# Kernel optimization log

Hardware: AMD Instinct MI355X
Metric: run time of the kernel (lower is better)

Reference implementation:

```python
import jax, jax.numpy as jnp
import numpy as np

N_ATOMS = 10000
N_EDGES = 250000
F_DIM = 128
N_RBF = 20
CUTOFF = 5.0
N_INT = 3
EPS = 1e-8


def setup_inputs() -> dict:
    key = jax.random.key(0)
    ks = jax.random.split(key, 16)
    inp = {}
    inp["atomic_numbers"] = jax.random.randint(ks[0], (N_ATOMS,), 1, 101)
    # positions in a 5 Angstrom box so many pairs lie inside the cutoff
    inp["R"] = jax.random.uniform(ks[1], (N_ATOMS, 3), dtype=jnp.float32) * 5.0
    idx_i = jnp.sort(jax.random.randint(ks[2], (N_EDGES,), 0, N_ATOMS))
    # ensure idx_j != idx_i so d_ij > 0
    idx_j = (idx_i + 1 + jax.random.randint(ks[3], (N_EDGES,), 0, N_ATOMS - 1)) % N_ATOMS
    inp["idx_i"] = idx_i
    inp["idx_j"] = idx_j
    inp["offsets"] = jnp.zeros((N_EDGES, 3), dtype=jnp.float32)

    def w(k, shape):
        fan_in = shape[-2]
        return jax.random.normal(k, shape, dtype=jnp.float32) / np.sqrt(fan_in).astype(np.float32)

    inp["emb"] = jax.random.normal(ks[4], (101, F_DIM), dtype=jnp.float32)
    inp["filt_W"] = w(ks[5], (N_RBF, 3 * F_DIM))
    inp["filt_b"] = jax.random.normal(ks[6], (3 * F_DIM,), dtype=jnp.float32) * 0.01
    inp["int_W1"] = w(ks[7], (N_INT, F_DIM, F_DIM))
    inp["int_b1"] = jnp.zeros((N_INT, 1, F_DIM), dtype=jnp.float32)
    inp["int_W2"] = w(ks[8], (N_INT, F_DIM, 3 * F_DIM))
    inp["int_b2"] = jnp.zeros((N_INT, 1, 3 * F_DIM), dtype=jnp.float32)
    inp["mix_Wmu"] = w(ks[9], (N_INT, F_DIM, 2 * F_DIM))
    inp["mix_W1"] = w(ks[10], (N_INT, 2 * F_DIM, F_DIM))
    inp["mix_b1"] = jnp.zeros((N_INT, 1, F_DIM), dtype=jnp.float32)
    inp["mix_W2"] = w(ks[11], (N_INT, F_DIM, 3 * F_DIM))
    inp["mix_b2"] = jnp.zeros((N_INT, 1, 3 * F_DIM), dtype=jnp.float32)
    return inp


def painn_forward(atomic_numbers, idx_i, idx_j, R, offsets, emb, filt_W, filt_b,
                  int_W1, int_b1, int_W2, int_b2,
                  mix_Wmu, mix_W1, mix_b1, mix_W2, mix_b2):
    n_atoms = atomic_numbers.shape[0]
    # geometry
    r_ij = R[idx_j] - R[idx_i] + offsets                      # [E,3]
    d_ij = jnp.linalg.norm(r_ij, axis=1, keepdims=True)       # [E,1]
    dir_ij = r_ij / d_ij                                      # [E,3]
    # Gaussian radial basis + cosine cutoff (schnetpack defaults)
    centers = jnp.linspace(0.0, CUTOFF, N_RBF, dtype=jnp.float32)
    coeff = -0.5 / (centers[1] - centers[0]) ** 2
    phi = jnp.exp(coeff * (d_ij[..., None] - centers) ** 2)   # [E,1,N_RBF]
    fcut = 0.5 * (jnp.cos(d_ij * (jnp.pi / CUTOFF)) + 1.0) * (d_ij < CUTOFF)  # [E,1]
    Wij = (phi @ filt_W + filt_b) * fcut[..., None]           # [E,1,3F] (shared filters)

    q = emb[atomic_numbers][:, None, :]                       # [N,1,F]
    mu = jnp.zeros((n_atoms, 3, F_DIM), dtype=q.dtype)        # [N,3,F]

    for i in range(N_INT):
        # ---- interaction (equivariant message passing) ----
        x = jax.nn.silu(q @ int_W1[i] + int_b1[i]) @ int_W2[i] + int_b2[i]  # [N,1,3F]
        xj = x[idx_j]                                          # [E,1,3F]
        muj = mu[idx_j]                                        # [E,3,F]
        xw = Wij * xj                                          # [E,1,3F]
        dq, dmuR, dmumu = jnp.split(xw, 3, axis=-1)            # each [E,1,F]
        dq = jax.ops.segment_sum(dq, idx_i, num_segments=n_atoms)          # [N,1,F]
        dmu = dmuR * dir_ij[..., None] + dmumu * muj           # [E,3,F]
        dmu = jax.ops.segment_sum(dmu, idx_i, num_segments=n_atoms)        # [N,3,F]
        q = q + dq
        mu = mu + dmu
        # ---- mixing (intra-atomic) ----
        mu_mix = mu @ mix_Wmu[i]                               # [N,3,2F]
        mu_V, mu_W = jnp.split(mu_mix, 2, axis=-1)             # [N,3,F] each
        mu_Vn = jnp.sqrt(jnp.sum(mu_V ** 2, axis=-2, keepdims=True) + EPS)  # [N,1,F]
        ctx = jnp.concatenate([q, mu_Vn], axis=-1)             # [N,1,2F]
        xm = jax.nn.silu(ctx @ mix_W1[i] + mix_b1[i]) @ mix_W2[i] + mix_b2[i]  # [N,1,3F]
        dq_intra, dmu_intra, dqmu_intra = jnp.split(xm, 3, axis=-1)
        dmu_intra = dmu_intra * mu_W                           # [N,3,F]
        dqmu_intra = dqmu_intra * jnp.sum(mu_V * mu_W, axis=1, keepdims=True)  # [N,1,F]
        q = q + dq_intra + dqmu_intra
        mu = mu + dmu_intra

    return q.squeeze(1), mu                                    # [N,F], [N,3,F]


def reference(atomic_numbers, R, idx_i, idx_j, offsets, emb, filt_W, filt_b,
              int_W1, int_b1, int_W2, int_b2,
              mix_Wmu, mix_W1, mix_b1, mix_W2, mix_b2):
    return painn_forward(atomic_numbers, idx_i, idx_j, R, offsets, emb, filt_W, filt_b,
                         int_W1, int_b1, int_W2, int_b2,
                         mix_Wmu, mix_W1, mix_b1, mix_W2, mix_b2)
```

## Files before the change

kernel.cpp:

```cpp
#include <hip/hip_runtime.h>
#include <math.h>

#define NA 10000
#define NE 250000
#define FD 128
#define NRBF 20
#define RCUT 5.0f

typedef _Float16 h16;
typedef __attribute__((ext_vector_type(8))) _Float16 half8;
typedef __attribute__((ext_vector_type(2))) _Float16 half2v;
typedef __attribute__((ext_vector_type(4))) float f32x4;

static __device__ __forceinline__ half8 f32x8_to_h8(const float* p) {
    float4 a = *(const float4*)p;
    float4 b = *(const float4*)(p + 4);
    half8 r;
    r[0] = (h16)a.x; r[1] = (h16)a.y; r[2] = (h16)a.z; r[3] = (h16)a.w;
    r[4] = (h16)b.x; r[5] = (h16)b.y; r[6] = (h16)b.z; r[7] = (h16)b.w;
    return r;
}
static __device__ __forceinline__ float silu(float v) {
    return v / (1.f + expf(-v));
}

__global__ __launch_bounds__(256) void setup_kernel(
    const float* __restrict__ R, const int* __restrict__ idx_i,
    const int* __restrict__ idx_j, const float* __restrict__ offsets,
    h16* __restrict__ ed, int* __restrict__ row_start,
    const float* __restrict__ int_W1, const float* __restrict__ int_W2,
    const float* __restrict__ mix_Wmu, const float* __restrict__ mix_W1,
    const float* __restrict__ mix_W2,
    h16* __restrict__ W1t, h16* __restrict__ W2t, h16* __restrict__ WmuT,
    h16* __restrict__ mW1t, h16* __restrict__ mW2t,
    const float* __restrict__ filt_W, const float* __restrict__ filt_b,
    h16* __restrict__ fwt)
{
    const int b = blockIdx.x;
    if (b < 977) {
        int e = b * 256 + threadIdx.x;
        if (e >= NE) return;
        int i = idx_i[e], j = idx_j[e];
        float rx = R[j * 3 + 0] - R[i * 3 + 0] + offsets[e * 3 + 0];
        float ry = R[j * 3 + 1] - R[i * 3 + 1] + offsets[e * 3 + 1];
        float rz = R[j * 3 + 2] - R[i * 3 + 2] + offsets[e * 3 + 2];
        float d = sqrtf(rx * rx + ry * ry + rz * rz);
        float inv = 1.f / d;
        float fcut = 0.f;
        if (d < RCUT) fcut = 0.5f * (cosf(d * (3.14159265358979323846f / RCUT)) + 1.f);
        h16* pp = ed + (size_t)e * 32;
        const float delta = RCUT / 19.f;
        const float coeff = -0.5f / (delta * delta);
#pragma unroll
        for (int r = 0; r < NRBF; ++r) {
            float dc = d - (float)r * delta;
            pp[r] = (h16)(expf(coeff * dc * dc) * fcut);
        }
        pp[20] = (h16)fcut;
        pp[21] = (h16)0.f; pp[22] = (h16)0.f; pp[23] = (h16)0.f;
        *(float4*)(pp + 24) = make_float4(rx * inv, ry * inv, rz * inv, 0.f);
    } else if (b < 1017) {
        int n = (b - 977) * 256 + threadIdx.x;
        if (n > NA) return;
        int lo = 0, hi = NE;
        while (lo < hi) {
            int mid = (lo + hi) >> 1;
            if (idx_i[mid] < n) lo = mid + 1; else hi = mid;
        }
        row_start[n] = lo;
    } else {
        int idx = (b - 1017) * 256 + threadIdx.x;
        if (idx < 49152) {
            int bt = idx >> 14, rem = idx & 16383;
            int nn = rem >> 7, kk = rem & 127;
            W1t[idx] = (h16)int_W1[(size_t)bt * 16384 + kk * 128 + nn];
        } else if ((idx -= 49152) < 147456) {
            int bt = idx / 49152, rem = idx - bt * 49152;
            int nn = rem >> 7, kk = rem & 127;
            W2t[idx] = (h16)int_W2[(size_t)bt * 49152 + kk * 384 + nn];
        } else if ((idx -= 147456) < 98304) {
            int bt = idx >> 15, rem = idx & 32767;
            int nn = rem >> 7, kk = rem & 127;
            WmuT[idx] = (h16)mix_Wmu[(size_t)bt * 32768 + kk * 256 + nn];
        } else if ((idx -= 98304) < 98304) {
            int bt = idx >> 15, rem = idx & 32767;
            int nn = rem >> 8, kk = rem & 255;
            mW1t[idx] = (h16)mix_W1[(size_t)bt * 32768 + kk * 128 + nn];
        } else if ((idx -= 98304) < 147456) {
            int bt = idx / 49152, rem = idx - bt * 49152;
            int nn = rem >> 7, kk = rem & 127;
            mW2t[idx] = (h16)mix_W2[(size_t)bt * 49152 + kk * 384 + nn];
        } else if ((idx -= 147456) < 12288) {
            int nn = idx >> 5, kk = idx & 31;
            float v = 0.f;
            if (kk < 20) v = filt_W[kk * 384 + nn];
            else if (kk == 20) v = filt_b[nn];
            fwt[idx] = (h16)v;
        }
    }
}

__global__ __launch_bounds__(256) void intmlp0_kernel(
    const int* __restrict__ Z, const float* __restrict__ emb, float* __restrict__ q,
    const h16* __restrict__ W1t, const float* __restrict__ b1,
    const h16* __restrict__ W2t, const float* __restrict__ b2, h16* __restrict__ x01c)
{
    __shared__ h16 Hs[16 * 136];
    const int tid = threadIdx.x;
    const int wave = tid >> 6, lane = tid & 63;
    const int ar = lane & 15, kg = lane >> 4;
    const size_t row0 = (size_t)blockIdx.x * 16;

    {
        int a = tid >> 4, f0 = (tid & 15) * 8;
        const float* src = emb + (size_t)Z[row0 + a] * 128 + f0;
        float4 v0 = *(const float4*)src;
        float4 v1 = *(const float4*)(src + 4);
        *(float4*)&q[(row0 + a) * 128 + f0] = v0;
        *(float4*)&q[(row0 + a) * 128 + f0 + 4] = v1;
    }
    const int zr = Z[row0 + ar];
    f32x4 a1[2] = {};
    for (int ks = 0; ks < 128; ks += 32) {
        int k = ks + kg * 8;
        half8 af = f32x8_to_h8(emb + (size_t)zr * 128 + k);
#pragma unroll
        for (int tt = 0; tt < 2; ++tt) {
            int t = wave * 2 + tt;
            half8 bf = *(const half8*)&W1t[(size_t)(t * 16 + ar) * 128 + k];
            a1[tt] = __builtin_amdgcn_mfma_f32_16x16x32_f16(af, bf, a1[tt], 0, 0, 0);
        }
    }
#pragma unroll
    for (int tt = 0; tt < 2; ++tt) {
        int col = (wave * 2 + tt) * 16 + ar;
        float bb = b1[col];
#pragma unroll
        for (int r = 0; r < 4; ++r)
            Hs[(kg * 4 + r) * 136 + col] = (h16)silu(a1[tt][r] + bb);
    }
    __syncthreads();
    f32x4 a2[6] = {};
    for (int ks = 0; ks < 128; ks += 32) {
        int k = ks + kg * 8;
        half8 af = *(const half8*)&Hs[ar * 136 + k];
#pragma unroll
        for (int tt = 0; tt < 6; ++tt) {
            int t = wave * 6 + tt;
            half8 bf = *(const half8*)&W2t[(size_t)(t * 16 + ar) * 128 + k];
            a2[tt] = __builtin_amdgcn_mfma_f32_16x16x32_f16(af, bf, a2[tt], 0, 0, 0);
        }
    }
#pragma unroll
    for (int tt = 0; tt < 6; ++tt) {
        int col = (wave * 6 + tt) * 16 + ar;
        if (col < 256) {
            float bb = b2[col];
            int slot = col >> 7, ff = col & 127;
#pragma unroll
            for (int r = 0; r < 4; ++r)
                x01c[((row0 + kg * 4 + r) * 128 + ff) * 2 + slot] = (h16)(a2[tt][r] + bb);
        }
    }
}

template<bool HAS_MU>
__global__ __launch_bounds__(128, 4) void edge_kernel(
    const h16* __restrict__ ed, const h16* __restrict__ fwt,
    const int* __restrict__ row_start, const int* __restrict__ idx_j,
    const h16* __restrict__ gat, const float* __restrict__ mup,
    float* __restrict__ mun, h16* __restrict__ mu16n, float* __restrict__ q)
{
    const int n = blockIdx.x, f = threadIdx.x;
    half8 FA[3], FB[3], FC[3];
    {
        const half8* pa = (const half8*)(fwt + (size_t)f * 32);
        const half8* pb = (const half8*)(fwt + (size_t)(128 + f) * 32);
#pragma unroll
        for (int r = 0; r < 3; ++r) { FA[r] = pa[r]; FB[r] = pb[r]; }
        if (HAS_MU) {
            const half8* pc = (const half8*)(fwt + (size_t)(256 + f) * 32);
#pragma unroll
            for (int r = 0; r < 3; ++r) FC[r] = pc[r];
        }
    }
    asm volatile("" : "+v"(FA[0]), "+v"(FA[1]), "+v"(FA[2]),
                      "+v"(FB[0]), "+v"(FB[1]), "+v"(FB[2]));
    if (HAS_MU)
        asm volatile("" : "+v"(FC[0]), "+v"(FC[1]), "+v"(FC[2]));

    half2v fa[12], fb[12], fc[12];
    *(half8*)&fa[0] = FA[0]; *(half8*)&fa[4] = FA[1]; *(half8*)&fa[8] = FA[2];
    *(half8*)&fb[0] = FB[0]; *(half8*)&fb[4] = FB[1]; *(half8*)&fb[8] = FB[2];
    if (HAS_MU) {
        *(half8*)&fc[0] = FC[0]; *(half8*)&fc[4] = FC[1]; *(half8*)&fc[8] = FC[2];
    }

    const size_t rstr = HAS_MU ? 768 : 256;
    const h16* xmf = gat + (HAS_MU ? (size_t)f * 6 : (size_t)f * 2);
    float accq = 0.f, am0 = 0.f, am1 = 0.f, am2 = 0.f;
    const int e0 = row_start[n], e1 = row_start[n + 1];
    if (e0 < e1) {
        int j = idx_j[e0];
        const unsigned* gp = (const unsigned*)(xmf + (size_t)j * rstr);
        unsigned g0n = gp[0], g1n = 0u, g2n = 0u;
        if (HAS_MU) { g1n = gp[1]; g2n = gp[2]; }
        const h16* pb8 = ed + (size_t)e0 * 32;
        half8 p0n = *(const half8*)pb8;
        half8 p1n = *(const half8*)(pb8 + 8);
        half8 p2n = *(const half8*)(pb8 + 16);
        float4 dn = *(const float4*)(pb8 + 24);
        for (int e = e0; e < e1; ++e) {
            unsigned g0 = g0n, g1 = g1n, g2 = g2n;
            half8 p0 = p0n, p1 = p1n, p2 = p2n;
            float4 g = dn;
            int ep = (e + 1 < e1) ? e + 1 : e;
            int j2 = idx_j[ep];
            const unsigned* gp2 = (const unsigned*)(xmf + (size_t)j2 * rstr);
            g0n = gp2[0];
            if (HAS_MU) { g1n = gp2[1]; g2n = gp2[2]; }
            const h16* pb2 = ed + (size_t)ep * 32;
            p0n = *(const half8*)pb2;
            p1n = *(const half8*)(pb2 + 8);
            p2n = *(const half8*)(pb2 + 16);
            dn = *(const float4*)(pb2 + 24);
            half2v pr[12];
            *(half8*)&pr[0] = p0; *(half8*)&pr[4] = p1; *(half8*)&pr[8] = p2;
            half2v A0 = {(h16)0.f, (h16)0.f}, A1 = A0, A2 = A0;
#pragma unroll
            for (int r = 0; r < 11; ++r) {
                A0 = pr[r] * fa[r] + A0;
                A1 = pr[r] * fb[r] + A1;
                if (HAS_MU) A2 = pr[r] * fc[r] + A2;
            }
            float w0 = (float)A0[0] + (float)A0[1];
            float w1 = (float)A1[0] + (float)A1[1];
            half2v h01 = __builtin_bit_cast(half2v, g0);
            half2v h23 = __builtin_bit_cast(half2v, g1);
            float x0 = (float)h01[0], x1 = (float)h01[1];
            accq = fmaf(w0, x0, accq);
            float xw1 = w1 * x1;
            if (HAS_MU) {
                float w2 = (float)A2[0] + (float)A2[1];
                half2v h45 = __builtin_bit_cast(half2v, g2);
                float x2 = (float)h23[0];
                float xw2 = w2 * x2;
                am0 += xw1 * g.x + xw2 * (float)h23[1];
                am1 += xw1 * g.y + xw2 * (float)h45[0];
                am2 += xw1 * g.z + xw2 * (float)h45[1];
            } else {
                am0 = fmaf(xw1, g.x, am0);
                am1 = fmaf(xw1, g.y, am1);
                am2 = fmaf(xw1, g.z, am2);
            }
        }
    }

    q[(size_t)n * FD + f] += accq;
    size_t b = (size_t)n * 384;
    float m0 = (HAS_MU ? mup[b + f] : 0.f) + am0;
    float m1 = (HAS_MU ? mup[b + 128 + f] : 0.f) + am1;
    float m2 = (HAS_MU ? mup[b + 256 + f] : 0.f) + am2;
    mun[b + f] = m0; mun[b + 128 + f] = m1; mun[b + 256 + f] = m2;
    mu16n[b + f] = (h16)m0; mu16n[b + 128 + f] = (h16)m1; mu16n[b + 256 + f] = (h16)m2;
}

__global__ __launch_bounds__(256) void mixint_kernel(
    const h16* __restrict__ mu16n, const h16* __restrict__ WmuT,
    const h16* __restrict__ W1t, const float* __restrict__ b1,
    const h16* __restrict__ W2t, const float* __restrict__ b2,
    float* __restrict__ q, float* __restrict__ mu, h16* __restrict__ xmw,
    const h16* __restrict__ nW1t, const float* __restrict__ nb1,
    const h16* __restrict__ nW2t, const float* __restrict__ nb2)
{
    __shared__ __align__(16) h16 MM[48 * 264];
    __shared__ h16 CT[16 * 264];
    __shared__ h16 Hs[16 * 136];
    __shared__ h16 XM[16 * 392];
    const int tid = threadIdx.x;
    const int wave = tid >> 6, lane = tid & 63;
    const int ar = lane & 15, kg = lane >> 4;
    const size_t row0 = (size_t)blockIdx.x * 16;

    {
        f32x4 acc[3][4] = {};
        int aloc[3], dloc[3];
#pragma unroll
        for (int rt = 0; rt < 3; ++rt) {
            int rr = rt * 16 + ar;
            aloc[rt] = rr / 3;
            dloc[rt] = rr - 3 * aloc[rt];
        }
        for (int ks = 0; ks < 128; ks += 32) {
            int k = ks + kg * 8;
            half8 afr[3];
#pragma unroll
            for (int rt = 0; rt < 3; ++rt)
                afr[rt] = *(const half8*)&mu16n[(row0 + aloc[rt]) * 384 + dloc[rt] * 128 + k];
#pragma unroll
            for (int ct = 0; ct < 4; ++ct) {
                int cc = wave * 4 + ct;
                half8 bf = *(const half8*)&WmuT[(size_t)(cc * 16 + ar) * 128 + k];
#pragma unroll
                for (int rt = 0; rt < 3; ++rt)
                    acc[rt][ct] = __builtin_amdgcn_mfma_f32_16x16x32_f16(afr[rt], bf, acc[rt][ct], 0, 0, 0);
            }
        }
#pragma unroll
        for (int rt = 0; rt < 3; ++rt)
#pragma unroll
            for (int ct = 0; ct < 4; ++ct) {
                int col = (wave * 4 + ct) * 16 + ar;
#pragma unroll
                for (int r = 0; r < 4; ++r)
                    MM[(rt * 16 + kg * 4 + r) * 264 + col] = (h16)acc[rt][ct][r];
            }
    }
    __syncthreads();

    {
        int a = tid >> 4, fi = (tid & 15) * 8;
        const float* qp = q + (row0 + a) * 128 + fi;
        float4 q0 = *(const float4*)qp;
        float4 q1 = *(const float4*)(qp + 4);
        float qv[8] = {q0.x, q0.y, q0.z, q0.w, q1.x, q1.y, q1.z, q1.w};
#pragma unroll
        for (int jj = 0; jj < 8; ++jj) {
            int ff = fi + jj;
            float v0 = (float)MM[(a * 3 + 0) * 264 + ff];
            float v1 = (float)MM[(a * 3 + 1) * 264 + ff];
            float v2 = (float)MM[(a * 3 + 2) * 264 + ff];
            CT[a * 264 + 128 + ff] = (h16)sqrtf(v0 * v0 + v1 * v1 + v2 * v2 + 1e-8f);
            CT[a * 264 + ff] = (h16)qv[jj];
        }
    }
    __syncthreads();

    {
        f32x4 a1[2] = {};
        for (int ks = 0; ks < 256; ks += 32) {
            int k = ks + kg * 8;
            half8 af = *(const half8*)&CT[ar * 264 + k];
#pragma unroll
            for (int tt = 0; tt < 2; ++tt) {
                int t = wave * 2 + tt;
                half8 bf = *(const half8*)&W1t[(size_t)(t * 16 + ar) * 256 + k];
                a1[tt] = __builtin_amdgcn_mfma_f32_16x16x32_f16(af, bf, a1[tt], 0, 0, 0);
            }
        }
#pragma unroll
        for (int tt = 0; tt < 2; ++tt) {
            int col = (wave * 2 + tt) * 16 + ar;
            float bb = b1[col];
#pragma unroll
            for (int r = 0; r < 4; ++r)
                Hs[(kg * 4 + r) * 136 + col] = (h16)silu(a1[tt][r] + bb);
        }
    }
    __syncthreads();

    {
        f32x4 a2[6] = {};
        for (int ks = 0; ks < 128; ks += 32) {
            int k = ks + kg * 8;
            half8 af = *(const half8*)&Hs[ar * 136 + k];
#pragma unroll
            for (int tt = 0; tt < 6; ++tt) {
                int t = wave * 6 + tt;
                half8 bf = *(const half8*)&W2t[(size_t)(t * 16 + ar) * 128 + k];
                a2[tt] = __builtin_amdgcn_mfma_f32_16x16x32_f16(af, bf, a2[tt], 0, 0, 0);
            }
        }
#pragma unroll
        for (int tt = 0; tt < 6; ++tt) {
            int col = (wave * 6 + tt) * 16 + ar;
            float bb = b2[col];
#pragma unroll
            for (int r = 0; r < 4; ++r)
                XM[(kg * 4 + r) * 392 + col] = (h16)(a2[tt][r] + bb);
        }
    }
    __syncthreads();

    h16 mh[24];
    {
        int a = tid >> 4, fi = (tid & 15) * 8;
        size_t n = row0 + a;
#pragma unroll
        for (int jj = 0; jj < 8; ++jj) {
            int ff = fi + jj;
            float dq  = (float)XM[a * 392 + ff];
            float dm  = (float)XM[a * 392 + 128 + ff];
            float dqm = (float)XM[a * 392 + 256 + ff];
            float v0 = (float)MM[(a * 3 + 0) * 264 + ff], w0 = (float)MM[(a * 3 + 0) * 264 + 128 + ff];
            float v1 = (float)MM[(a * 3 + 1) * 264 + ff], w1 = (float)MM[(a * 3 + 1) * 264 + 128 + ff];
            float v2 = (float)MM[(a * 3 + 2) * 264 + ff], w2 = (float)MM[(a * 3 + 2) * 264 + 128 + ff];
            float sv = v0 * w0 + v1 * w1 + v2 * w2;
            float qn = q[n * 128 + ff] + dq + dqm * sv;
            q[n * 128 + ff] = qn;
            CT[a * 264 + ff] = (h16)qn;
            size_t b = n * 384 + ff;
            float m0 = mu[b] + dm * w0;
            float m1 = mu[b + 128] + dm * w1;
            float m2 = mu[b + 256] + dm * w2;
            mu[b] = m0; mu[b + 128] = m1; mu[b + 256] = m2;
            mh[jj * 3 + 0] = (h16)m0; mh[jj * 3 + 1] = (h16)m1; mh[jj * 3 + 2] = (h16)m2;
        }
    }
    if (!nW1t) return;
    __syncthreads();

    {
        f32x4 a1[2] = {};
        for (int ks = 0; ks < 128; ks += 32) {
            int k = ks + kg * 8;
            half8 af = *(const half8*)&CT[ar * 264 + k];
#pragma unroll
            for (int tt = 0; tt < 2; ++tt) {
                int t = wave * 2 + tt;
                half8 bf = *(const half8*)&nW1t[(size_t)(t * 16 + ar) * 128 + k];
                a1[tt] = __builtin_amdgcn_mfma_f32_16x16x32_f16(af, bf, a1[tt], 0, 0, 0);
            }
        }
#pragma unroll
        for (int tt = 0; tt < 2; ++tt) {
            int col = (wave * 2 + tt) * 16 + ar;
            float bb = nb1[col];
#pragma unroll
            for (int r = 0; r < 4; ++r)
                Hs[(kg * 4 + r) * 136 + col] = (h16)silu(a1[tt][r] + bb);
        }
        __syncthreads();
        f32x4 a2[6] = {};
        for (int ks = 0; ks < 128; ks += 32) {
            int k = ks + kg * 8;
            half8 af = *(const half8*)&Hs[ar * 136 + k];
#pragma unroll
            for (int tt = 0; tt < 6; ++tt) {
                int t = wave * 6 + tt;
                half8 bf = *(const half8*)&nW2t[(size_t)(t * 16 + ar) * 128 + k];
                a2[tt] = __builtin_amdgcn_mfma_f32_16x16x32_f16(af, bf, a2[tt], 0, 0, 0);
            }
        }
        h16* XMP = MM;
#pragma unroll
        for (int tt = 0; tt < 6; ++tt) {
            int col = (wave * 6 + tt) * 16 + ar;
            float bb = nb2[col];
            int slot = col >> 7, ff = col & 127;
#pragma unroll
            for (int r = 0; r < 4; ++r)
                XMP[((kg * 4 + r) * 128 + ff) * 6 + slot] = (h16)(a2[tt][r] + bb);
        }
        {
            int a = tid >> 4, fi = (tid & 15) * 8;
#pragma unroll
            for (int jj = 0; jj < 8; ++jj)
#pragma unroll
                for (int s = 0; s < 3; ++s)
                    XMP[(a * 128 + fi + jj) * 6 + 3 + s] = mh[jj * 3 + s];
        }
        __syncthreads();
        {
            const uint4* src = (const uint4*)MM;
            uint4* dst = (uint4*)(xmw + row0 * 768);
#pragma unroll
            for (int i = 0; i < 6; ++i)
                dst[tid + i * 256] = src[tid + i * 256];
        }
    }
}

extern "C" void kernel_launch(void* const* d_in, const int* in_sizes, int n_in,
                              void* d_out, int out_size, void* d_ws, size_t ws_size,
                              hipStream_t stream)
{
    const int*   Z       = (const int*)d_in[0];
    const float* R       = (const float*)d_in[1];
    const int*   idx_i   = (const int*)d_in[2];
    const int*   idx_j   = (const int*)d_in[3];
    const float* offsets = (const float*)d_in[4];
    const float* emb     = (const float*)d_in[5];
    const float* filt_W  = (const float*)d_in[6];
    const float* filt_b  = (const float*)d_in[7];
    const float* int_W1  = (const float*)d_in[8];
    const float* int_b1  = (const float*)d_in[9];
    const float* int_W2  = (const float*)d_in[10];
    const float* int_b2  = (const float*)d_in[11];
    const float* mix_Wmu = (const float*)d_in[12];
    const float* mix_W1  = (const float*)d_in[13];
    const float* mix_b1  = (const float*)d_in[14];
    const float* mix_W2  = (const float*)d_in[15];
    const float* mix_b2  = (const float*)d_in[16];

    float* q_out  = (float*)d_out;
    float* mu_out = (float*)d_out + (size_t)NA * FD;

    char* base = (char*)d_ws;
    size_t o = 0;
    auto alloc = [&](size_t bytes) -> void* {
        void* p = base + o;
        o += (bytes + 255) & ~(size_t)255;
        return p;
    };
    h16*   ed     = (h16*)alloc((size_t)NE * 32 * 2);
    h16*   xm     = (h16*)alloc((size_t)NA * 128 * 6 * 2);
    h16*   x01c   = (h16*)alloc((size_t)NA * 128 * 2 * 2);
    h16*   mu16p  = (h16*)alloc((size_t)NA * 384 * 2);
    float* mu_ws  = (float*)alloc((size_t)NA * 384 * 4);
    h16*   W1t    = (h16*)alloc((size_t)3 * 128 * 128 * 2);
    h16*   W2t    = (h16*)alloc((size_t)3 * 384 * 128 * 2);
    h16*   WmuT   = (h16*)alloc((size_t)3 * 256 * 128 * 2);
    h16*   mW1t   = (h16*)alloc((size_t)3 * 128 * 256 * 2);
    h16*   mW2t   = (h16*)alloc((size_t)3 * 384 * 128 * 2);
    h16*   fwt    = (h16*)alloc((size_t)384 * 32 * 2);
    int*   row_st = (int*)alloc((size_t)(NA + 1) * 4);

    setup_kernel<<<3177, 256, 0, stream>>>(R, idx_i, idx_j, offsets, ed, row_st,
                                           int_W1, int_W2, mix_Wmu, mix_W1, mix_W2,
                                           W1t, W2t, WmuT, mW1t, mW2t,
                                           filt_W, filt_b, fwt);

    intmlp0_kernel<<<NA / 16, 256, 0, stream>>>(Z, emb, q_out,
                                                W1t, int_b1, W2t, int_b2, x01c);
    edge_kernel<false><<<NA, 128, 0, stream>>>(ed, fwt, row_st, idx_j,
                                               x01c, nullptr, mu_out, mu16p, q_out);
    mixint_kernel<<<NA / 16, 256, 0, stream>>>(
        mu16p, WmuT, mW1t, mix_b1, mW2t, mix_b2, q_out, mu_out, xm,
        W1t + 16384, int_b1 + 128, W2t + 49152, int_b2 + 384);

    edge_kernel<true><<<NA, 128, 0, stream>>>(ed, fwt, row_st, idx_j,
                                              xm, mu_out, mu_ws, mu16p, q_out);
    mixint_kernel<<<NA / 16, 256, 0, stream>>>(
        mu16p, WmuT + 32768, mW1t + 32768, mix_b1 + 128, mW2t + 49152, mix_b2 + 384,
        q_out, mu_ws, xm,
        W1t + 32768, int_b1 + 256, W2t + 98304, int_b2 + 768);

    edge_kernel<true><<<NA, 128, 0, stream>>>(ed, fwt, row_st, idx_j,
                                              xm, mu_ws, mu_out, mu16p, q_out);
    mixint_kernel<<<NA / 16, 256, 0, stream>>>(
        mu16p, WmuT + 65536, mW1t + 65536, mix_b1 + 256, mW2t + 98304, mix_b2 + 768,
        q_out, mu_out, xm,
        nullptr, nullptr, nullptr, nullptr);
}
```

Before: 424.8 us.

## Compute first interaction MLP per element type instead of per atom

In the first interaction block the features depend only on atomic number, so the MLP now runs over the 101 embedding rows rather than all 10000 atoms. The neighbour's atomic number is packed into a spare slot of the per-edge record, so the first edge pass indexes the small per-type table directly without reading idx_j. The q initialisation moves into the setup kernel, and the mixing kernel reuses q values already held in registers instead of reloading them. This removes most of the first MLP's work and cuts gather traffic, at the cost of a more tangled setup kernel and an fp16 bit-cast trick to store an integer.

```diff
diff --git a/kernel.cpp b/kernel.cpp
--- a/kernel.cpp
+++ b/kernel.cpp
@@ -27,6 +27,7 @@
 __global__ __launch_bounds__(256) void setup_kernel(
     const float* __restrict__ R, const int* __restrict__ idx_i,
     const int* __restrict__ idx_j, const float* __restrict__ offsets,
+    const int* __restrict__ Zt, const float* __restrict__ emb, float* __restrict__ q,
     h16* __restrict__ ed, int* __restrict__ row_start,
     const float* __restrict__ int_W1, const float* __restrict__ int_W2,
     const float* __restrict__ mix_Wmu, const float* __restrict__ mix_W1,
@@ -57,7 +58,9 @@
             pp[r] = (h16)(expf(coeff * dc * dc) * fcut);
         }
         pp[20] = (h16)fcut;
-        pp[21] = (h16)0.f; pp[22] = (h16)0.f; pp[23] = (h16)0.f;
+        pp[21] = (h16)0.f;
+        pp[22] = __builtin_bit_cast(h16, (unsigned short)Zt[j]);
+        pp[23] = (h16)0.f;
         *(float4*)(pp + 24) = make_float4(rx * inv, ry * inv, rz * inv, 0.f);
     } else if (b < 1017) {
         int n = (b - 977) * 256 + threadIdx.x;
@@ -68,7 +71,7 @@
             if (idx_i[mid] < n) lo = mid + 1; else hi = mid;
         }
         row_start[n] = lo;
-    } else {
+    } else if (b < 3177) {
         int idx = (b - 1017) * 256 + threadIdx.x;
         if (idx < 49152) {
             int bt = idx >> 14, rem = idx & 16383;
@@ -97,29 +100,31 @@
             else if (kk == 20) v = filt_b[nn];
             fwt[idx] = (h16)v;
         }
-    }
-}
-
-__global__ __launch_bounds__(256) void intmlp0_kernel(
-    const int* __restrict__ Z, const float* __restrict__ emb, float* __restrict__ q,
+    } else {
+        int a = (b - 3177) * 16 + (threadIdx.x >> 4);
+        int f0 = (threadIdx.x & 15) * 8;
+        if (a < NA) {
+            const float* src = emb + (size_t)Zt[a] * 128 + f0;
+            float4 v0 = *(const float4*)src;
+            float4 v1 = *(const float4*)(src + 4);
+            *(float4*)&q[(size_t)a * 128 + f0] = v0;
+            *(float4*)&q[(size_t)a * 128 + f0 + 4] = v1;
+        }
+    }
+}
+
+__global__ __launch_bounds__(256) void intmlp0z_kernel(
+    const float* __restrict__ emb,
     const h16* __restrict__ W1t, const float* __restrict__ b1,
-    const h16* __restrict__ W2t, const float* __restrict__ b2, h16* __restrict__ x01c)
+    const h16* __restrict__ W2t, const float* __restrict__ b2, h16* __restrict__ x01z)
 {
     __shared__ h16 Hs[16 * 136];
     const int tid = threadIdx.x;
     const int wave = tid >> 6, lane = tid & 63;
     const int ar = lane & 15, kg = lane >> 4;
-    const size_t row0 = (size_t)blockIdx.x * 16;
-
-    {
-        int a = tid >> 4, f0 = (tid & 15) * 8;
-        const float* src = emb + (size_t)Z[row0 + a] * 128 + f0;
-        float4 v0 = *(const float4*)src;
-        float4 v1 = *(const float4*)(src + 4);
-        *(float4*)&q[(row0 + a) * 128 + f0] = v0;
-        *(float4*)&q[(row0 + a) * 128 + f0 + 4] = v1;
-    }
-    const int zr = Z[row0 + ar];
+    const int row0 = blockIdx.x * 16;
+
+    const int zr = min(row0 + ar, 100);
     f32x4 a1[2] = {};
     for (int ks = 0; ks < 128; ks += 32) {
         int k = ks + kg * 8;
@@ -158,8 +163,11 @@
             float bb = b2[col];
             int slot = col >> 7, ff = col & 127;
 #pragma unroll
-            for (int r = 0; r < 4; ++r)
-                x01c[((row0 + kg * 4 + r) * 128 + ff) * 2 + slot] = (h16)(a2[tt][r] + bb);
+            for (int r = 0; r < 4; ++r) {
+                int z = row0 + kg * 4 + r;
+                if (z <= 100)
+                    x01z[((size_t)z * 128 + ff) * 2 + slot] = (h16)(a2[tt][r] + bb);
+            }
         }
     }
 }
@@ -196,59 +204,94 @@
         *(half8*)&fc[0] = FC[0]; *(half8*)&fc[4] = FC[1]; *(half8*)&fc[8] = FC[2];
     }
 
-    const size_t rstr = HAS_MU ? 768 : 256;
-    const h16* xmf = gat + (HAS_MU ? (size_t)f * 6 : (size_t)f * 2);
     float accq = 0.f, am0 = 0.f, am1 = 0.f, am2 = 0.f;
     const int e0 = row_start[n], e1 = row_start[n + 1];
-    if (e0 < e1) {
-        int j = idx_j[e0];
-        const unsigned* gp = (const unsigned*)(xmf + (size_t)j * rstr);
-        unsigned g0n = gp[0], g1n = 0u, g2n = 0u;
-        if (HAS_MU) { g1n = gp[1]; g2n = gp[2]; }
-        const h16* pb8 = ed + (size_t)e0 * 32;
-        half8 p0n = *(const half8*)pb8;
-        half8 p1n = *(const half8*)(pb8 + 8);
-        half8 p2n = *(const half8*)(pb8 + 16);
-        float4 dn = *(const float4*)(pb8 + 24);
-        for (int e = e0; e < e1; ++e) {
-            unsigned g0 = g0n, g1 = g1n, g2 = g2n;
-            half8 p0 = p0n, p1 = p1n, p2 = p2n;
-            float4 g = dn;
-            int ep = (e + 1 < e1) ? e + 1 : e;
-            int j2 = idx_j[ep];
-            const unsigned* gp2 = (const unsigned*)(xmf + (size_t)j2 * rstr);
-            g0n = gp2[0];
-            if (HAS_MU) { g1n = gp2[1]; g2n = gp2[2]; }
-            const h16* pb2 = ed + (size_t)ep * 32;
-            p0n = *(const half8*)pb2;
-            p1n = *(const half8*)(pb2 + 8);
-            p2n = *(const half8*)(pb2 + 16);
-            dn = *(const float4*)(pb2 + 24);
-            half2v pr[12];
-            *(half8*)&pr[0] = p0; *(half8*)&pr[4] = p1; *(half8*)&pr[8] = p2;
-            half2v A0 = {(h16)0.f, (h16)0.f}, A1 = A0, A2 = A0;
-#pragma unroll
-            for (int r = 0; r < 11; ++r) {
-                A0 = pr[r] * fa[r] + A0;
-                A1 = pr[r] * fb[r] + A1;
-                if (HAS_MU) A2 = pr[r] * fc[r] + A2;
-            }
-            float w0 = (float)A0[0] + (float)A0[1];
-            float w1 = (float)A1[0] + (float)A1[1];
-            half2v h01 = __builtin_bit_cast(half2v, g0);
-            half2v h23 = __builtin_bit_cast(half2v, g1);
-            float x0 = (float)h01[0], x1 = (float)h01[1];
-            accq = fmaf(w0, x0, accq);
-            float xw1 = w1 * x1;
-            if (HAS_MU) {
+
+    if (HAS_MU) {
+        const h16* xmf = gat + (size_t)f * 6;
+        if (e0 < e1) {
+            int j = idx_j[e0];
+            const unsigned* gp = (const unsigned*)(xmf + (size_t)j * 768);
+            unsigned g0n = gp[0], g1n = gp[1], g2n = gp[2];
+            const h16* pb8 = ed + (size_t)e0 * 32;
+            half8 p0n = *(const half8*)pb8;
+            half8 p1n = *(const half8*)(pb8 + 8);
+            half8 p2n = *(const half8*)(pb8 + 16);
+            float4 dn = *(const float4*)(pb8 + 24);
+            for (int e = e0; e < e1; ++e) {
+                unsigned g0 = g0n, g1 = g1n, g2 = g2n;
+                half8 p0 = p0n, p1 = p1n, p2 = p2n;
+                float4 g = dn;
+                int ep = (e + 1 < e1) ? e + 1 : e;
+                int j2 = idx_j[ep];
+                const unsigned* gp2 = (const unsigned*)(xmf + (size_t)j2 * 768);
+                g0n = gp2[0]; g1n = gp2[1]; g2n = gp2[2];
+                const h16* pb2 = ed + (size_t)ep * 32;
+                p0n = *(const half8*)pb2;
+                p1n = *(const half8*)(pb2 + 8);
+                p2n = *(const half8*)(pb2 + 16);
+                dn = *(const float4*)(pb2 + 24);
+                half2v pr[12];
+                *(half8*)&pr[0] = p0; *(half8*)&pr[4] = p1; *(half8*)&pr[8] = p2;
+                half2v A0 = {(h16)0.f, (h16)0.f}, A1 = A0, A2 = A0;
+#pragma unroll
+                for (int r = 0; r < 11; ++r) {
+                    A0 = pr[r] * fa[r] + A0;
+                    A1 = pr[r] * fb[r] + A1;
+                    A2 = pr[r] * fc[r] + A2;
+                }
+                float w0 = (float)A0[0] + (float)A0[1];
+                float w1 = (float)A1[0] + (float)A1[1];
                 float w2 = (float)A2[0] + (float)A2[1];
+                half2v h01 = __builtin_bit_cast(half2v, g0);
+                half2v h23 = __builtin_bit_cast(half2v, g1);
                 half2v h45 = __builtin_bit_cast(half2v, g2);
+                float x0 = (float)h01[0], x1 = (float)h01[1];
+                accq = fmaf(w0, x0, accq);
+                float xw1 = w1 * x1;
                 float x2 = (float)h23[0];
                 float xw2 = w2 * x2;
                 am0 += xw1 * g.x + xw2 * (float)h23[1];
                 am1 += xw1 * g.y + xw2 * (float)h45[0];
                 am2 += xw1 * g.z + xw2 * (float)h45[1];
-            } else {
+            }
+        }
+    } else {
+        const h16* xmf = gat + (size_t)f * 2;
+        if (e0 < e1) {
+            const h16* pb8 = ed + (size_t)e0 * 32;
+            half8 p0n = *(const half8*)pb8;
+            half8 p1n = *(const half8*)(pb8 + 8);
+            half8 p2n = *(const half8*)(pb8 + 16);
+            float4 dn = *(const float4*)(pb8 + 24);
+            unsigned short z0 = __builtin_bit_cast(unsigned short, (h16)p2n[6]);
+            unsigned g0n = *(const unsigned*)(xmf + (size_t)z0 * 256);
+            for (int e = e0; e < e1; ++e) {
+                unsigned g0 = g0n;
+                half8 p0 = p0n, p1 = p1n, p2 = p2n;
+                float4 g = dn;
+                int ep = (e + 1 < e1) ? e + 1 : e;
+                const h16* pb2 = ed + (size_t)ep * 32;
+                p0n = *(const half8*)pb2;
+                p1n = *(const half8*)(pb2 + 8);
+                p2n = *(const half8*)(pb2 + 16);
+                dn = *(const float4*)(pb2 + 24);
+                unsigned short z2 = __builtin_bit_cast(unsigned short, (h16)p2n[6]);
+                g0n = *(const unsigned*)(xmf + (size_t)z2 * 256);
+                half2v pr[12];
+                *(half8*)&pr[0] = p0; *(half8*)&pr[4] = p1; *(half8*)&pr[8] = p2;
+                half2v A0 = {(h16)0.f, (h16)0.f}, A1 = A0;
+#pragma unroll
+                for (int r = 0; r < 11; ++r) {
+                    A0 = pr[r] * fa[r] + A0;
+                    A1 = pr[r] * fb[r] + A1;
+                }
+                float w0 = (float)A0[0] + (float)A0[1];
+                float w1 = (float)A1[0] + (float)A1[1];
+                half2v h01 = __builtin_bit_cast(half2v, g0);
+                float x0 = (float)h01[0], x1 = (float)h01[1];
+                accq = fmaf(w0, x0, accq);
+                float xw1 = w1 * x1;
                 am0 = fmaf(xw1, g.x, am0);
                 am1 = fmaf(xw1, g.y, am1);
                 am2 = fmaf(xw1, g.z, am2);
@@ -318,12 +361,14 @@
     }
     __syncthreads();
 
+    float qv[8];
     {
         int a = tid >> 4, fi = (tid & 15) * 8;
         const float* qp = q + (row0 + a) * 128 + fi;
         float4 q0 = *(const float4*)qp;
         float4 q1 = *(const float4*)(qp + 4);
-        float qv[8] = {q0.x, q0.y, q0.z, q0.w, q1.x, q1.y, q1.z, q1.w};
+        qv[0] = q0.x; qv[1] = q0.y; qv[2] = q0.z; qv[3] = q0.w;
+        qv[4] = q1.x; qv[5] = q1.y; qv[6] = q1.z; qv[7] = q1.w;
 #pragma unroll
         for (int jj = 0; jj < 8; ++jj) {
             int ff = fi + jj;
@@ -396,7 +441,7 @@
             float v1 = (float)MM[(a * 3 + 1) * 264 + ff], w1 = (float)MM[(a * 3 + 1) * 264 + 128 + ff];
             float v2 = (float)MM[(a * 3 + 2) * 264 + ff], w2 = (float)MM[(a * 3 + 2) * 264 + 128 + ff];
             float sv = v0 * w0 + v1 * w1 + v2 * w2;
-            float qn = q[n * 128 + ff] + dq + dqm * sv;
+            float qn = qv[jj] + dq + dqm * sv;
             q[n * 128 + ff] = qn;
             CT[a * 264 + ff] = (h16)qn;
             size_t b = n * 384 + ff;
@@ -505,7 +550,7 @@
     };
     h16*   ed     = (h16*)alloc((size_t)NE * 32 * 2);
     h16*   xm     = (h16*)alloc((size_t)NA * 128 * 6 * 2);
-    h16*   x01c   = (h16*)alloc((size_t)NA * 128 * 2 * 2);
+    h16*   x01z   = (h16*)alloc((size_t)101 * 128 * 2 * 2);
     h16*   mu16p  = (h16*)alloc((size_t)NA * 384 * 2);
     float* mu_ws  = (float*)alloc((size_t)NA * 384 * 4);
     h16*   W1t    = (h16*)alloc((size_t)3 * 128 * 128 * 2);
@@ -516,15 +561,15 @@
     h16*   fwt    = (h16*)alloc((size_t)384 * 32 * 2);
     int*   row_st = (int*)alloc((size_t)(NA + 1) * 4);
 
-    setup_kernel<<<3177, 256, 0, stream>>>(R, idx_i, idx_j, offsets, ed, row_st,
+    setup_kernel<<<3802, 256, 0, stream>>>(R, idx_i, idx_j, offsets, Z, emb, q_out,
+                                           ed, row_st,
                                            int_W1, int_W2, mix_Wmu, mix_W1, mix_W2,
                                            W1t, W2t, WmuT, mW1t, mW2t,
                                            filt_W, filt_b, fwt);
 
-    intmlp0_kernel<<<NA / 16, 256, 0, stream>>>(Z, emb, q_out,
-                                                W1t, int_b1, W2t, int_b2, x01c);
+    intmlp0z_kernel<<<7, 256, 0, stream>>>(emb, W1t, int_b1, W2t, int_b2, x01z);
     edge_kernel<false><<<NA, 128, 0, stream>>>(ed, fwt, row_st, idx_j,
-                                               x01c, nullptr, mu_out, mu16p, q_out);
+                                               x01z, nullptr, mu_out, mu16p, q_out);
     mixint_kernel<<<NA / 16, 256, 0, stream>>>(
         mu16p, WmuT, mW1t, mix_b1, mW2t, mix_b2, q_out, mu_out, xm,
         W1t + 16384, int_b1 + 128, W2t + 49152, int_b2 + 384);
```

Result: no change. 418.4 us (-1.5%).

## Compute first interaction MLP per element type and gather by atomic number

Applied to the files above, without the earlier changes.

In the first interaction the MLP input is just the embedding of each atom's type, so the MLP now runs over the 101 possible atomic numbers instead of all atoms. The edge kernel gathers the result through a per-edge 16-bit atomic-number index built in setup. The q embedding copy moves into the setup kernel, the edge loop prefetches neighbour indices two edges ahead, and mixint reuses q values it already holds in registers instead of reloading them. The cost is a small extra per-edge index array and an extra dependent Z lookup during setup.

```diff
diff --git a/kernel.cpp b/kernel.cpp
--- a/kernel.cpp
+++ b/kernel.cpp
@@ -27,7 +27,8 @@
 __global__ __launch_bounds__(256) void setup_kernel(
     const float* __restrict__ R, const int* __restrict__ idx_i,
     const int* __restrict__ idx_j, const float* __restrict__ offsets,
-    h16* __restrict__ ed, int* __restrict__ row_start,
+    const int* __restrict__ Zt, const float* __restrict__ emb, float* __restrict__ q,
+    h16* __restrict__ ed, unsigned short* __restrict__ zs, int* __restrict__ row_start,
     const float* __restrict__ int_W1, const float* __restrict__ int_W2,
     const float* __restrict__ mix_Wmu, const float* __restrict__ mix_W1,
     const float* __restrict__ mix_W2,
@@ -59,6 +60,7 @@
         pp[20] = (h16)fcut;
         pp[21] = (h16)0.f; pp[22] = (h16)0.f; pp[23] = (h16)0.f;
         *(float4*)(pp + 24) = make_float4(rx * inv, ry * inv, rz * inv, 0.f);
+        zs[e] = (unsigned short)Zt[j];
     } else if (b < 1017) {
         int n = (b - 977) * 256 + threadIdx.x;
         if (n > NA) return;
@@ -68,7 +70,7 @@
             if (idx_i[mid] < n) lo = mid + 1; else hi = mid;
         }
         row_start[n] = lo;
-    } else {
+    } else if (b < 3177) {
         int idx = (b - 1017) * 256 + threadIdx.x;
         if (idx < 49152) {
             int bt = idx >> 14, rem = idx & 16383;
@@ -97,29 +99,31 @@
             else if (kk == 20) v = filt_b[nn];
             fwt[idx] = (h16)v;
         }
-    }
-}
-
-__global__ __launch_bounds__(256) void intmlp0_kernel(
-    const int* __restrict__ Z, const float* __restrict__ emb, float* __restrict__ q,
+    } else {
+        int a = (b - 3177) * 16 + (threadIdx.x >> 4);
+        int f0 = (threadIdx.x & 15) * 8;
+        if (a < NA) {
+            const float* src = emb + (size_t)Zt[a] * 128 + f0;
+            float4 v0 = *(const float4*)src;
+            float4 v1 = *(const float4*)(src + 4);
+            *(float4*)&q[(size_t)a * 128 + f0] = v0;
+            *(float4*)&q[(size_t)a * 128 + f0 + 4] = v1;
+        }
+    }
+}
+
+__global__ __launch_bounds__(256) void intmlp0z_kernel(
+    const float* __restrict__ emb,
     const h16* __restrict__ W1t, const float* __restrict__ b1,
-    const h16* __restrict__ W2t, const float* __restrict__ b2, h16* __restrict__ x01c)
+    const h16* __restrict__ W2t, const float* __restrict__ b2, h16* __restrict__ x01z)
 {
     __shared__ h16 Hs[16 * 136];
     const int tid = threadIdx.x;
     const int wave = tid >> 6, lane = tid & 63;
     const int ar = lane & 15, kg = lane >> 4;
-    const size_t row0 = (size_t)blockIdx.x * 16;
-
-    {
-        int a = tid >> 4, f0 = (tid & 15) * 8;
-        const float* src = emb + (size_t)Z[row0 + a] * 128 + f0;
-        float4 v0 = *(const float4*)src;
-        float4 v1 = *(const float4*)(src + 4);
-        *(float4*)&q[(row0 + a) * 128 + f0] = v0;
-        *(float4*)&q[(row0 + a) * 128 + f0 + 4] = v1;
-    }
-    const int zr = Z[row0 + ar];
+    const int row0 = blockIdx.x * 16;
+
+    const int zr = min(row0 + ar, 100);
     f32x4 a1[2] = {};
     for (int ks = 0; ks < 128; ks += 32) {
         int k = ks + kg * 8;
@@ -158,8 +162,11 @@
             float bb = b2[col];
             int slot = col >> 7, ff = col & 127;
 #pragma unroll
-            for (int r = 0; r < 4; ++r)
-                x01c[((row0 + kg * 4 + r) * 128 + ff) * 2 + slot] = (h16)(a2[tt][r] + bb);
+            for (int r = 0; r < 4; ++r) {
+                int z = row0 + kg * 4 + r;
+                if (z <= 100)
+                    x01z[((size_t)z * 128 + ff) * 2 + slot] = (h16)(a2[tt][r] + bb);
+            }
         }
     }
 }
@@ -168,6 +175,7 @@
 __global__ __launch_bounds__(128, 4) void edge_kernel(
     const h16* __restrict__ ed, const h16* __restrict__ fwt,
     const int* __restrict__ row_start, const int* __restrict__ idx_j,
+    const unsigned short* __restrict__ zs,
     const h16* __restrict__ gat, const float* __restrict__ mup,
     float* __restrict__ mun, h16* __restrict__ mu16n, float* __restrict__ q)
 {
@@ -200,11 +208,19 @@
     const h16* xmf = gat + (HAS_MU ? (size_t)f * 6 : (size_t)f * 2);
     float accq = 0.f, am0 = 0.f, am1 = 0.f, am2 = 0.f;
     const int e0 = row_start[n], e1 = row_start[n + 1];
+
+#define LD_IDX(E) (HAS_MU ? idx_j[E] : (int)zs[E])
+
     if (e0 < e1) {
-        int j = idx_j[e0];
-        const unsigned* gp = (const unsigned*)(xmf + (size_t)j * rstr);
+        const int elast = e1 - 1;
+        int j0 = LD_IDX(e0);
+        const unsigned* gp = (const unsigned*)(xmf + (size_t)j0 * rstr);
         unsigned g0n = gp[0], g1n = 0u, g2n = 0u;
         if (HAS_MU) { g1n = gp[1]; g2n = gp[2]; }
+        int eA = (e0 + 1 < elast) ? e0 + 1 : elast;
+        int eB = (e0 + 2 < elast) ? e0 + 2 : elast;
+        int jA = LD_IDX(eA);
+        int jB = LD_IDX(eB);
         const h16* pb8 = ed + (size_t)e0 * 32;
         half8 p0n = *(const half8*)pb8;
         half8 p1n = *(const half8*)(pb8 + 8);
@@ -214,11 +230,13 @@
             unsigned g0 = g0n, g1 = g1n, g2 = g2n;
             half8 p0 = p0n, p1 = p1n, p2 = p2n;
             float4 g = dn;
-            int ep = (e + 1 < e1) ? e + 1 : e;
-            int j2 = idx_j[ep];
-            const unsigned* gp2 = (const unsigned*)(xmf + (size_t)j2 * rstr);
+            const unsigned* gp2 = (const unsigned*)(xmf + (size_t)jA * rstr);
             g0n = gp2[0];
             if (HAS_MU) { g1n = gp2[1]; g2n = gp2[2]; }
+            jA = jB;
+            int e3 = (e + 3 < elast) ? e + 3 : elast;
+            jB = LD_IDX(e3);
+            int ep = (e + 1 < e1) ? e + 1 : e;
             const h16* pb2 = ed + (size_t)ep * 32;
             p0n = *(const half8*)pb2;
             p1n = *(const half8*)(pb2 + 8);
@@ -255,6 +273,7 @@
             }
         }
     }
+#undef LD_IDX
 
     q[(size_t)n * FD + f] += accq;
     size_t b = (size_t)n * 384;
@@ -318,12 +337,14 @@
     }
     __syncthreads();
 
+    float qv[8];
     {
         int a = tid >> 4, fi = (tid & 15) * 8;
         const float* qp = q + (row0 + a) * 128 + fi;
         float4 q0 = *(const float4*)qp;
         float4 q1 = *(const float4*)(qp + 4);
-        float qv[8] = {q0.x, q0.y, q0.z, q0.w, q1.x, q1.y, q1.z, q1.w};
+        qv[0] = q0.x; qv[1] = q0.y; qv[2] = q0.z; qv[3] = q0.w;
+        qv[4] = q1.x; qv[5] = q1.y; qv[6] = q1.z; qv[7] = q1.w;
 #pragma unroll
         for (int jj = 0; jj < 8; ++jj) {
             int ff = fi + jj;
@@ -396,7 +417,7 @@
             float v1 = (float)MM[(a * 3 + 1) * 264 + ff], w1 = (float)MM[(a * 3 + 1) * 264 + 128 + ff];
             float v2 = (float)MM[(a * 3 + 2) * 264 + ff], w2 = (float)MM[(a * 3 + 2) * 264 + 128 + ff];
             float sv = v0 * w0 + v1 * w1 + v2 * w2;
-            float qn = q[n * 128 + ff] + dq + dqm * sv;
+            float qn = qv[jj] + dq + dqm * sv;
             q[n * 128 + ff] = qn;
             CT[a * 264 + ff] = (h16)qn;
             size_t b = n * 384 + ff;
@@ -504,8 +525,9 @@
         return p;
     };
     h16*   ed     = (h16*)alloc((size_t)NE * 32 * 2);
+    unsigned short* zs = (unsigned short*)alloc((size_t)NE * 2);
     h16*   xm     = (h16*)alloc((size_t)NA * 128 * 6 * 2);
-    h16*   x01c   = (h16*)alloc((size_t)NA * 128 * 2 * 2);
+    h16*   x01z   = (h16*)alloc((size_t)101 * 128 * 2 * 2);
     h16*   mu16p  = (h16*)alloc((size_t)NA * 384 * 2);
     float* mu_ws  = (float*)alloc((size_t)NA * 384 * 4);
     h16*   W1t    = (h16*)alloc((size_t)3 * 128 * 128 * 2);
@@ -516,27 +538,27 @@
     h16*   fwt    = (h16*)alloc((size_t)384 * 32 * 2);
     int*   row_st = (int*)alloc((size_t)(NA + 1) * 4);
 
-    setup_kernel<<<3177, 256, 0, stream>>>(R, idx_i, idx_j, offsets, ed, row_st,
+    setup_kernel<<<3802, 256, 0, stream>>>(R, idx_i, idx_j, offsets, Z, emb, q_out,
+                                           ed, zs, row_st,
                                            int_W1, int_W2, mix_Wmu, mix_W1, mix_W2,
                                            W1t, W2t, WmuT, mW1t, mW2t,
                                            filt_W, filt_b, fwt);
 
-    intmlp0_kernel<<<NA / 16, 256, 0, stream>>>(Z, emb, q_out,
-                                                W1t, int_b1, W2t, int_b2, x01c);
-    edge_kernel<false><<<NA, 128, 0, stream>>>(ed, fwt, row_st, idx_j,
-                                               x01c, nullptr, mu_out, mu16p, q_out);
+    intmlp0z_kernel<<<7, 256, 0, stream>>>(emb, W1t, int_b1, W2t, int_b2, x01z);
+    edge_kernel<false><<<NA, 128, 0, stream>>>(ed, fwt, row_st, idx_j, zs,
+                                               x01z, nullptr, mu_out, mu16p, q_out);
     mixint_kernel<<<NA / 16, 256, 0, stream>>>(
         mu16p, WmuT, mW1t, mix_b1, mW2t, mix_b2, q_out, mu_out, xm,
         W1t + 16384, int_b1 + 128, W2t + 49152, int_b2 + 384);
 
-    edge_kernel<true><<<NA, 128, 0, stream>>>(ed, fwt, row_st, idx_j,
+    edge_kernel<true><<<NA, 128, 0, stream>>>(ed, fwt, row_st, idx_j, zs,
                                               xm, mu_out, mu_ws, mu16p, q_out);
     mixint_kernel<<<NA / 16, 256, 0, stream>>>(
         mu16p, WmuT + 32768, mW1t + 32768, mix_b1 + 128, mW2t + 49152, mix_b2 + 384,
         q_out, mu_ws, xm,
         W1t + 32768, int_b1 + 256, W2t + 98304, int_b2 + 768);
 
-    edge_kernel<true><<<NA, 128, 0, stream>>>(ed, fwt, row_st, idx_j,
+    edge_kernel<true><<<NA, 128, 0, stream>>>(ed, fwt, row_st, idx_j, zs,
                                               xm, mu_ws, mu_out, mu16p, q_out);
     mixint_kernel<<<NA / 16, 256, 0, stream>>>(
         mu16p, WmuT + 65536, mW1t + 65536, mix_b1 + 256, mW2t + 98304, mix_b2 + 768,
```

Measured after the change: 431.0 us. Within noise of the previous version (+1.5%).
